# Optimization experiments

Measured on AMD Instinct MI355X. Metric: run time of the kernel, lower is better.

Reference implementation:

```python
import jax, jax.numpy as jnp
import numpy as np

B, S, D, E, H = 4, 2048, 1024, 8, 4096

def setup_inputs() -> dict:
    key = jax.random.key(0)
    ks = jax.random.split(key, 7)
    scale_d = 1.0 / np.sqrt(D)
    scale_h = 1.0 / np.sqrt(H)
    return {
        "x": jax.random.normal(ks[0], (B, S, D), dtype=jnp.float32),
        "Wr": jax.random.uniform(ks[1], (D, E), jnp.float32, -scale_d, scale_d),
        "br": jnp.zeros((E,), jnp.float32),
        "W1": jax.random.uniform(ks[2], (E, D, H), jnp.float32, -scale_d, scale_d),
        "b1": jax.random.uniform(ks[3], (E, H), jnp.float32, -scale_d, scale_d),
        "W2": jax.random.uniform(ks[4], (E, H, D), jnp.float32, -scale_h, scale_h),
        "b2": jax.random.uniform(ks[5], (E, D), jnp.float32, -scale_h, scale_h),
    }

def reference(x, Wr, br, W1, b1, W2, b2):
    # Router: softmax then argmax (top-1). Note: original does NOT scale
    # expert output by the routing weight and never applies capacity drop.
    route_logits = jnp.einsum("bsd,de->bse", x, Wr) + br
    routing_weights = jax.nn.softmax(route_logits, axis=-1)
    selected_expert = jnp.argmax(routing_weights, axis=-1)  # [B, S] int

    num_experts = W1.shape[0]
    out = jnp.zeros_like(x)
    # Fixed small loop over experts (structurally distinct weight slices);
    # select-by-mask keeps shapes static under jit.
    for e in range(num_experts):
        h = jax.nn.gelu(jnp.einsum("bsd,dh->bsh", x, W1[e]) + b1[e], approximate=False)
        y = jnp.einsum("bsh,hd->bsd", h, W2[e]) + b2[e]
        out = jnp.where((selected_expert == e)[..., None], y, out)
    return out
```

## Files before the change

### kernel.cpp

```cpp
#include <hip/hip_runtime.h>
#include <math.h>

#define TOK   8192
#define DD    1024
#define EE    8
#define HH    4096
#define MAXROWS 9216
#define MAXMT 72

typedef unsigned short u16;
typedef unsigned int   u32;
typedef __bf16 bf16x8 __attribute__((ext_vector_type(8)));
typedef float  f32x16 __attribute__((ext_vector_type(16)));

__device__ __forceinline__ u16 f2bf(float f) {
  union { float f; u32 u; } v; v.f = f;
  u32 r = v.u + 0x7fffu + ((v.u >> 16) & 1u);
  return (u16)(r >> 16);
}

__device__ __forceinline__ void gload16(const void* g, void* l) {
  __builtin_amdgcn_global_load_lds(
      (const __attribute__((address_space(1))) void*)g,
      (__attribute__((address_space(3))) void*)l, 16, 0, 0);
}

__global__ void k_init(int* rowmap, int* counts, int* fill) {
  int i = blockIdx.x * 256 + threadIdx.x;
  if (i < MAXROWS) rowmap[i] = -1;
  if (blockIdx.x == 0 && threadIdx.x < EE) { counts[threadIdx.x] = 0; fill[threadIdx.x] = 0; }
}

__global__ __launch_bounds__(256)
void k_route(const float* __restrict__ x, const float* __restrict__ Wr,
             const float* __restrict__ br, int* __restrict__ eid,
             int* __restrict__ counts, u16* __restrict__ xb) {
  int t = blockIdx.x * 4 + (threadIdx.x >> 6);
  int lt = threadIdx.x & 63;
  const float4* xr = (const float4*)(x + (size_t)t * DD);
  u16* xbr = xb + (size_t)t * DD;
  const float4* wrp = (const float4*)Wr;
  float acc[EE];
  #pragma unroll
  for (int e = 0; e < EE; ++e) acc[e] = 0.f;
  #pragma unroll
  for (int i = 0; i < 4; ++i) {
    int d4 = lt + 64 * i;
    float4 v = xr[d4];
    u32 p0 = (u32)f2bf(v.x) | ((u32)f2bf(v.y) << 16);
    u32 p1 = (u32)f2bf(v.z) | ((u32)f2bf(v.w) << 16);
    ((uint2*)xbr)[d4] = make_uint2(p0, p1);
    float vv[4] = { v.x, v.y, v.z, v.w };
    #pragma unroll
    for (int dd = 0; dd < 4; ++dd) {
      float xv = vv[dd];
      float4 a = wrp[(size_t)(d4 * 4 + dd) * 2];
      float4 b = wrp[(size_t)(d4 * 4 + dd) * 2 + 1];
      acc[0] += xv * a.x; acc[1] += xv * a.y; acc[2] += xv * a.z; acc[3] += xv * a.w;
      acc[4] += xv * b.x; acc[5] += xv * b.y; acc[6] += xv * b.z; acc[7] += xv * b.w;
    }
  }
  #pragma unroll
  for (int e = 0; e < EE; ++e)
    #pragma unroll
    for (int off = 32; off > 0; off >>= 1) acc[e] += __shfl_down(acc[e], off);
  if (lt == 0) {
    float best = -1e30f; int be = 0;
    #pragma unroll
    for (int e = 0; e < EE; ++e) {
      float v = acc[e] + br[e];
      if (v > best) { best = v; be = e; }
    }
    eid[t] = be;
    atomicAdd(&counts[be], 1);
  }
}

__global__ void k_scan(const int* __restrict__ counts, int* __restrict__ poff) {
  if (threadIdx.x == 0) {
    int off = 0; poff[0] = 0;
    for (int e = 0; e < EE; ++e) { off += ((counts[e] + 127) >> 7) << 7; poff[e + 1] = off; }
  }
}

__global__ void k_fillmap(const int* __restrict__ eid, const int* __restrict__ poff,
                          int* __restrict__ fill, int* __restrict__ rowmap) {
  int t = blockIdx.x * 256 + threadIdx.x;
  if (t < TOK) {
    int e = eid[t];
    int pos = atomicAdd(&fill[e], 1);
    rowmap[poff[e] + pos] = t;
  }
}

__global__ __launch_bounds__(256)
void k_transpose(const float* __restrict__ W, u16* __restrict__ WT, int K, int N) {
  __shared__ float tile[64][65];
  int e = blockIdx.z;
  int n0 = blockIdx.x * 64, k0 = blockIdx.y * 64;
  const float* We = W + (size_t)e * K * N;
  u16* WTe = WT + (size_t)e * K * N;
  int tx = threadIdx.x & 15, ty = threadIdx.x >> 4;
  #pragma unroll
  for (int i = 0; i < 4; ++i) {
    int r = ty + 16 * i;
    float4 v = *(const float4*)&We[(size_t)(k0 + r) * N + n0 + tx * 4];
    tile[r][tx * 4 + 0] = v.x; tile[r][tx * 4 + 1] = v.y;
    tile[r][tx * 4 + 2] = v.z; tile[r][tx * 4 + 3] = v.w;
  }
  __syncthreads();
  #pragma unroll
  for (int i = 0; i < 4; ++i) {
    int n = ty + 16 * i;
    ushort4 o;
    o.x = f2bf(tile[tx * 4 + 0][n]); o.y = f2bf(tile[tx * 4 + 1][n]);
    o.z = f2bf(tile[tx * 4 + 2][n]); o.w = f2bf(tile[tx * 4 + 3][n]);
    *(ushort4*)&WTe[(size_t)(n0 + n) * K + k0 + tx * 4] = o;
  }
}

template <int KDIM, int NDIM, bool G2, int KSPLIT>
__global__ __launch_bounds__(256, 3)
void k_gemm(const u16* __restrict__ Abase, const u16* __restrict__ WT,
            const float* __restrict__ bias, const int* __restrict__ poff,
            const int* __restrict__ rowmap, u16* __restrict__ hout,
            float* __restrict__ yout) {
  const int mbase = blockIdx.y * 128;
  if (mbase >= poff[EE]) return;
  int e = 0;
  #pragma unroll
  for (int q = 1; q < EE; ++q) e += (mbase >= poff[q]) ? 1 : 0;
  const int nbase = blockIdx.x * 128;
  const int koff = blockIdx.z * (KDIM / KSPLIT);
  constexpr int KT = KDIM / (32 * KSPLIT);

  const int tid = threadIdx.x;
  const int w = tid >> 6, lt = tid & 63;
  const int wr = w >> 1, wc = w & 1;

  __shared__ u16 ls[3][2][4096];

  const int rl0 = (w * 4 + 0 + (lt >> 5)) * 8 + (lt & 7);
  const int rl1 = (w * 4 + 2 + (lt >> 5)) * 8 + (lt & 7);
  const int ck = (lt >> 3) & 3;
  int arow0, arow1;
  if (G2) { arow0 = mbase + rl0; arow1 = mbase + rl1; }
  else {
    arow0 = rowmap[mbase + rl0]; if (arow0 < 0) arow0 = 0;
    arow1 = rowmap[mbase + rl1]; if (arow1 < 0) arow1 = 0;
  }
  const u16* gA0 = Abase + (size_t)arow0 * KDIM + koff + ck * 8;
  const u16* gA1 = Abase + (size_t)arow1 * KDIM + koff + ck * 8;
  const u16* wte = WT + (size_t)e * NDIM * KDIM + koff;
  const u16* gB0 = wte + (size_t)(nbase + rl0) * KDIM + ck * 8;
  const u16* gB1 = wte + (size_t)(nbase + rl1) * KDIM + ck * 8;

  #define STAGE(bi, ko)                                   \
    do {                                                  \
      gload16(gA0 + (ko), &ls[bi][0][(w * 128) * 8]);     \
      gload16(gA1 + (ko), &ls[bi][0][(w * 128 + 64) * 8]);\
      gload16(gB0 + (ko), &ls[bi][1][(w * 128) * 8]);     \
      gload16(gB1 + (ko), &ls[bi][1][(w * 128 + 64) * 8]);\
    } while (0)

  f32x16 acc[2][2] = {};
  STAGE(0, 0);
  STAGE(1, 32);

  int sbuf = 2, cbuf = 0;
  for (int bk = 0; bk < KT; ++bk) {
    if (bk + 1 < KT) asm volatile("s_waitcnt vmcnt(4) lgkmcnt(0)\ns_barrier" ::: "memory");
    else             asm volatile("s_waitcnt vmcnt(0) lgkmcnt(0)\ns_barrier" ::: "memory");
    if (bk + 2 < KT) STAGE(sbuf, (bk + 2) * 32);
    const u16* A = ls[cbuf][0];
    const u16* B = ls[cbuf][1];
    #pragma unroll
    for (int s = 0; s < 2; ++s) {
      const int cc = s * 2 + (lt >> 5);
      bf16x8 af[2], bg[2];
      #pragma unroll
      for (int i = 0; i < 2; ++i) {
        int r = wr * 64 + i * 32 + (lt & 31);
        int slot = ((r >> 3) << 5) + cc * 8 + (r & 7);
        af[i] = *(const bf16x8*)&A[slot * 8];
      }
      #pragma unroll
      for (int j = 0; j < 2; ++j) {
        int n = wc * 64 + j * 32 + (lt & 31);
        int slot = ((n >> 3) << 5) + cc * 8 + (n & 7);
        bg[j] = *(const bf16x8*)&B[slot * 8];
      }
      #pragma unroll
      for (int i = 0; i < 2; ++i)
        #pragma unroll
        for (int j = 0; j < 2; ++j)
          acc[i][j] = __builtin_amdgcn_mfma_f32_32x32x16_bf16(af[i], bg[j], acc[i][j], 0, 0, 0);
    }
    cbuf = (cbuf == 2) ? 0 : cbuf + 1;
    sbuf = (sbuf == 2) ? 0 : sbuf + 1;
  }
  #undef STAGE

  if (G2) {
    float* yo = yout + (size_t)blockIdx.z * ((size_t)TOK * DD);
    #pragma unroll
    for (int i = 0; i < 2; ++i) {
      const int rbase = wr * 64 + i * 32 + 4 * (lt >> 5);
      #pragma unroll
      for (int r = 0; r < 16; ++r) {
        const int rl = rbase + (r & 3) + 8 * (r >> 2);
        int tok = rowmap[mbase + rl];
        if (tok >= 0) {
          float* yp = yo + (size_t)tok * NDIM + nbase + wc * 64 + (lt & 31);
          #pragma unroll
          for (int j = 0; j < 2; ++j) yp[j * 32] = acc[i][j][r];
        }
      }
    }
  } else {
    float bv[2];
    #pragma unroll
    for (int j = 0; j < 2; ++j)
      bv[j] = bias[(size_t)e * NDIM + nbase + wc * 64 + j * 32 + (lt & 31)];
    #pragma unroll
    for (int i = 0; i < 2; ++i) {
      const int rbase = wr * 64 + i * 32 + 4 * (lt >> 5);
      #pragma unroll
      for (int r = 0; r < 16; ++r) {
        const int rl = rbase + (r & 3) + 8 * (r >> 2);
        u16* hp = hout + (size_t)(mbase + rl) * NDIM + nbase + wc * 64 + (lt & 31);
        #pragma unroll
        for (int j = 0; j < 2; ++j) {
          float v = acc[i][j][r] + bv[j];
          v = 0.5f * v * (1.0f + erff(v * 0.70710678118654752f));
          hp[j * 32] = f2bf(v);
        }
      }
    }
  }
}

__global__ void k_reduce(const float* __restrict__ p0, const float* __restrict__ p1,
                         const float* __restrict__ b2, const int* __restrict__ eid,
                         float* __restrict__ out) {
  int i = blockIdx.x * 256 + threadIdx.x;
  int tok = i >> 8;
  int d4 = i & 255;
  int e = eid[tok];
  float4 b = ((const float4*)(b2 + (size_t)e * DD))[d4];
  float4 a0 = ((const float4*)p0)[i];
  float4 a1 = ((const float4*)p1)[i];
  ((float4*)out)[i] = make_float4(b.x + a0.x + a1.x, b.y + a0.y + a1.y,
                                  b.z + a0.z + a1.z, b.w + a0.w + a1.w);
}

extern "C" void kernel_launch(void* const* d_in, const int* in_sizes, int n_in,
                              void* d_out, int out_size, void* d_ws, size_t ws_size,
                              hipStream_t stream) {
  const float* x  = (const float*)d_in[0];
  const float* Wr = (const float*)d_in[1];
  const float* br = (const float*)d_in[2];
  const float* W1 = (const float*)d_in[3];
  const float* b1 = (const float*)d_in[4];
  const float* W2 = (const float*)d_in[5];
  const float* b2 = (const float*)d_in[6];
  float* out = (float*)d_out;

  char* ws = (char*)d_ws;
  int* eid    = (int*)(ws + 0);
  int* counts = (int*)(ws + 32768);
  int* fill   = (int*)(ws + 32768 + 64);
  int* poff   = (int*)(ws + 32768 + 128);
  int* rowmap = (int*)(ws + 33024);
  u16* xbf    = (u16*)(ws + 69888);
  u16* w1t    = (u16*)(ws + 16847104);
  u16* w2t    = (u16*)(ws + 83955968);
  u16* hbuf   = (u16*)(ws + 151064832);
  float* pbuf = (float*)w1t;

  k_init<<<MAXROWS / 256, 256, 0, stream>>>(rowmap, counts, fill);
  k_route<<<TOK / 4, 256, 0, stream>>>(x, Wr, br, eid, counts, xbf);
  k_scan<<<1, 64, 0, stream>>>(counts, poff);
  k_fillmap<<<TOK / 256, 256, 0, stream>>>(eid, poff, fill, rowmap);
  k_transpose<<<dim3(HH / 64, DD / 64, EE), 256, 0, stream>>>(W1, w1t, DD, HH);
  k_transpose<<<dim3(DD / 64, HH / 64, EE), 256, 0, stream>>>(W2, w2t, HH, DD);
  k_gemm<DD, HH, false, 1><<<dim3(HH / 128, MAXMT, 1), 256, 0, stream>>>(xbf, w1t, b1, poff, rowmap, hbuf, nullptr);
  k_gemm<HH, DD, true, 2><<<dim3(DD / 128, MAXMT, 2), 256, 0, stream>>>(hbuf, w2t, nullptr, poff, rowmap, nullptr, pbuf);
  k_reduce<<<TOK * DD / 1024, 256, 0, stream>>>(pbuf, pbuf + (size_t)TOK * DD, b2, eid, out);
}
```

Measured before the change: 793.5 us.

## Remap GEMM blocks to XCDs and switch to double-buffered LDS with higher occupancy

Flattens the GEMM grid to 1D and decodes the block id so that blocks sharing the same weight column tile land on the same XCD (id & 7), aiming to improve L2 reuse of expert weights. The LDS pipeline drops from triple to double buffering with a plain __syncthreads, which frees shared memory so launch bounds can rise from 3 to 4 blocks per CU. The trade-off is a shallower prefetch depth, since only one stage is in flight while computing, which can expose more global-load latency.

```diff
diff --git a/kernel.cpp b/kernel.cpp
--- a/kernel.cpp
+++ b/kernel.cpp
@@ -119,26 +119,31 @@
   }
 }
 
-template <int KDIM, int NDIM, bool G2, int KSPLIT>
-__global__ __launch_bounds__(256, 3)
+template <int KDIM, int NDIM, bool G2>
+__global__ __launch_bounds__(256, 4)
 void k_gemm(const u16* __restrict__ Abase, const u16* __restrict__ WT,
             const float* __restrict__ bias, const int* __restrict__ poff,
             const int* __restrict__ rowmap, u16* __restrict__ hout,
             float* __restrict__ yout) {
-  const int mbase = blockIdx.y * 128;
+  const int id = blockIdx.x;
+  const int xcd = id & 7, j = id >> 3;
+  int nt, mt, z;
+  if (G2) { nt = xcd; mt = j >> 1; z = j & 1; }
+  else    { nt = xcd * 4 + (j & 3); mt = j >> 2; z = 0; }
+  const int mbase = mt * 128;
   if (mbase >= poff[EE]) return;
   int e = 0;
   #pragma unroll
   for (int q = 1; q < EE; ++q) e += (mbase >= poff[q]) ? 1 : 0;
-  const int nbase = blockIdx.x * 128;
-  const int koff = blockIdx.z * (KDIM / KSPLIT);
-  constexpr int KT = KDIM / (32 * KSPLIT);
+  const int nbase = nt * 128;
+  const int koff = G2 ? z * (KDIM / 2) : 0;
+  const int KT = G2 ? KDIM / 64 : KDIM / 32;
 
   const int tid = threadIdx.x;
   const int w = tid >> 6, lt = tid & 63;
   const int wr = w >> 1, wc = w & 1;
 
-  __shared__ u16 ls[3][2][4096];
+  __shared__ u16 ls[2][2][4096];
 
   const int rl0 = (w * 4 + 0 + (lt >> 5)) * 8 + (lt & 7);
   const int rl1 = (w * 4 + 2 + (lt >> 5)) * 8 + (lt & 7);
@@ -165,15 +170,11 @@
 
   f32x16 acc[2][2] = {};
   STAGE(0, 0);
-  STAGE(1, 32);
-
-  int sbuf = 2, cbuf = 0;
   for (int bk = 0; bk < KT; ++bk) {
-    if (bk + 1 < KT) asm volatile("s_waitcnt vmcnt(4) lgkmcnt(0)\ns_barrier" ::: "memory");
-    else             asm volatile("s_waitcnt vmcnt(0) lgkmcnt(0)\ns_barrier" ::: "memory");
-    if (bk + 2 < KT) STAGE(sbuf, (bk + 2) * 32);
-    const u16* A = ls[cbuf][0];
-    const u16* B = ls[cbuf][1];
+    __syncthreads();
+    if (bk + 1 < KT) STAGE((bk + 1) & 1, (bk + 1) * 32);
+    const u16* A = ls[bk & 1][0];
+    const u16* B = ls[bk & 1][1];
     #pragma unroll
     for (int s = 0; s < 2; ++s) {
       const int cc = s * 2 + (lt >> 5);
@@ -185,24 +186,22 @@
         af[i] = *(const bf16x8*)&A[slot * 8];
       }
       #pragma unroll
-      for (int j = 0; j < 2; ++j) {
-        int n = wc * 64 + j * 32 + (lt & 31);
+      for (int jj = 0; jj < 2; ++jj) {
+        int n = wc * 64 + jj * 32 + (lt & 31);
         int slot = ((n >> 3) << 5) + cc * 8 + (n & 7);
-        bg[j] = *(const bf16x8*)&B[slot * 8];
+        bg[jj] = *(const bf16x8*)&B[slot * 8];
       }
       #pragma unroll
       for (int i = 0; i < 2; ++i)
         #pragma unroll
-        for (int j = 0; j < 2; ++j)
-          acc[i][j] = __builtin_amdgcn_mfma_f32_32x32x16_bf16(af[i], bg[j], acc[i][j], 0, 0, 0);
-    }
-    cbuf = (cbuf == 2) ? 0 : cbuf + 1;
-    sbuf = (sbuf == 2) ? 0 : sbuf + 1;
+        for (int jj = 0; jj < 2; ++jj)
+          acc[i][jj] = __builtin_amdgcn_mfma_f32_32x32x16_bf16(af[i], bg[jj], acc[i][jj], 0, 0, 0);
+    }
   }
   #undef STAGE
 
   if (G2) {
-    float* yo = yout + (size_t)blockIdx.z * ((size_t)TOK * DD);
+    float* yo = yout + (size_t)z * ((size_t)TOK * DD);
     #pragma unroll
     for (int i = 0; i < 2; ++i) {
       const int rbase = wr * 64 + i * 32 + 4 * (lt >> 5);
@@ -213,15 +212,15 @@
         if (tok >= 0) {
           float* yp = yo + (size_t)tok * NDIM + nbase + wc * 64 + (lt & 31);
           #pragma unroll
-          for (int j = 0; j < 2; ++j) yp[j * 32] = acc[i][j][r];
+          for (int jj = 0; jj < 2; ++jj) yp[jj * 32] = acc[i][jj][r];
         }
       }
     }
   } else {
     float bv[2];
     #pragma unroll
-    for (int j = 0; j < 2; ++j)
-      bv[j] = bias[(size_t)e * NDIM + nbase + wc * 64 + j * 32 + (lt & 31)];
+    for (int jj = 0; jj < 2; ++jj)
+      bv[jj] = bias[(size_t)e * NDIM + nbase + wc * 64 + jj * 32 + (lt & 31)];
     #pragma unroll
     for (int i = 0; i < 2; ++i) {
       const int rbase = wr * 64 + i * 32 + 4 * (lt >> 5);
@@ -230,10 +229,10 @@
         const int rl = rbase + (r & 3) + 8 * (r >> 2);
         u16* hp = hout + (size_t)(mbase + rl) * NDIM + nbase + wc * 64 + (lt & 31);
         #pragma unroll
-        for (int j = 0; j < 2; ++j) {
-          float v = acc[i][j][r] + bv[j];
+        for (int jj = 0; jj < 2; ++jj) {
+          float v = acc[i][jj][r] + bv[jj];
           v = 0.5f * v * (1.0f + erff(v * 0.70710678118654752f));
-          hp[j * 32] = f2bf(v);
+          hp[jj * 32] = f2bf(v);
         }
       }
     }
@@ -284,7 +283,7 @@
   k_fillmap<<<TOK / 256, 256, 0, stream>>>(eid, poff, fill, rowmap);
   k_transpose<<<dim3(HH / 64, DD / 64, EE), 256, 0, stream>>>(W1, w1t, DD, HH);
   k_transpose<<<dim3(DD / 64, HH / 64, EE), 256, 0, stream>>>(W2, w2t, HH, DD);
-  k_gemm<DD, HH, false, 1><<<dim3(HH / 128, MAXMT, 1), 256, 0, stream>>>(xbf, w1t, b1, poff, rowmap, hbuf, nullptr);
-  k_gemm<HH, DD, true, 2><<<dim3(DD / 128, MAXMT, 2), 256, 0, stream>>>(hbuf, w2t, nullptr, poff, rowmap, nullptr, pbuf);
+  k_gemm<DD, HH, false><<<32 * MAXMT, 256, 0, stream>>>(xbf, w1t, b1, poff, rowmap, hbuf, nullptr);
+  k_gemm<HH, DD, true><<<8 * MAXMT * 2, 256, 0, stream>>>(hbuf, w2t, nullptr, poff, rowmap, nullptr, pbuf);
   k_reduce<<<TOK * DD / 1024, 256, 0, stream>>>(pbuf, pbuf + (size_t)TOK * DD, b2, eid, out);
 }
```

Result: no change. 790.6 us (-0.4%).
